# Optimization experiments

Hardware: AMD Instinct MI355X
Metric: run time of the kernel (lower is better)

## Reference

```python
import jax, jax.numpy as jnp
import numpy as np

B, S, D, H, NH, C = 32, 512, 768, 768, 4, 10
HD = H // NH


def _lin(x, w, b):
    return x @ w.T + b


def _ln(x, g, b, eps=1e-5):
    mu = jnp.mean(x, axis=-1, keepdims=True)
    var = jnp.mean(jnp.square(x - mu), axis=-1, keepdims=True)
    return (x - mu) * jax.lax.rsqrt(var + eps) * g + b


def setup_inputs() -> dict:
    key = jax.random.key(0)
    ks = jax.random.split(key, 16)
    w = lambda k, shape: jax.random.normal(k, shape, dtype=jnp.float32) * 0.02
    return {
        "x": jax.random.normal(ks[0], (B, S, D), dtype=jnp.float32),
        "wq": w(ks[1], (H, D)), "bq": jnp.zeros((H,), jnp.float32),
        "wk": w(ks[2], (H, D)), "bk": jnp.zeros((H,), jnp.float32),
        "wv": w(ks[3], (H, D)), "bv": jnp.zeros((H,), jnp.float32),
        "wx": w(ks[4], (H, D)), "bx": jnp.zeros((H,), jnp.float32),
        "in_proj_w": w(ks[5], (3 * H, H)), "in_proj_b": jnp.zeros((3 * H,), jnp.float32),
        "out_proj_w": w(ks[6], (H, H)), "out_proj_b": jnp.zeros((H,), jnp.float32),
        "fc1a_w": w(ks[7], (H, H)), "fc1a_b": jnp.zeros((H,), jnp.float32),
        "fc1b_w": w(ks[8], (H, H)), "fc1b_b": jnp.zeros((H,), jnp.float32),
        "ln_g": jnp.ones((H,), jnp.float32), "ln_b": jnp.zeros((H,), jnp.float32),
        "fc2_w": w(ks[9], (C, H)), "fc2_b": jnp.zeros((C,), jnp.float32),
    }


def reference(x, wq, bq, wk, bk, wv, bv, wx, bx, in_proj_w, in_proj_b,
              out_proj_w, out_proj_b, fc1a_w, fc1a_b, fc1b_w, fc1b_b,
              ln_g, ln_b, fc2_w, fc2_b):
    # Vectorized sinusoidal PE matching the triple loop:
    # even i: sin(pos / 10000^(2i/D)); odd i: cos(pos / 10000^(2(i-1)/D))
    d = x.shape[2]
    pos = jnp.arange(x.shape[1], dtype=x.dtype)[:, None]          # [S,1]
    i = jnp.arange(d)
    i_even = (i - (i % 2)).astype(x.dtype)                        # 2*(i - i%2)/d exponent
    angle = pos / jnp.power(jnp.asarray(10000.0, x.dtype), 2.0 * i_even / d)  # [S,D]
    pe = jnp.where(i % 2 == 0, jnp.sin(angle), jnp.cos(angle))
    x = x + pe[None]

    q = _lin(x, wq, bq)
    k = _lin(x, wk, bk)
    v = _lin(x, wv, bv)
    xr = _lin(x, wx, bx)

    # torch MultiheadAttention: in_proj, split heads, SDPA, out_proj
    wq_i, wk_i, wv_i = jnp.split(in_proj_w, 3, axis=0)
    bq_i, bk_i, bv_i = jnp.split(in_proj_b, 3, axis=0)
    b = x.shape[0]
    q2 = _lin(q, wq_i, bq_i).reshape(b, -1, NH, HD)
    k2 = _lin(k, wk_i, bk_i).reshape(b, -1, NH, HD)
    v2 = _lin(v, wv_i, bv_i).reshape(b, -1, NH, HD)
    scores = jnp.einsum('bqhd,bkhd->bhqk', q2, k2) / jnp.sqrt(jnp.asarray(HD, x.dtype))
    attn = jax.nn.softmax(scores, axis=-1)
    ctx = jnp.einsum('bhqk,bkhd->bqhd', attn, v2).reshape(b, -1, H)
    attn_out = _lin(ctx, out_proj_w, out_proj_b)

    x = _ln(xr + attn_out, ln_g, ln_b)
    ffn = _lin(jax.nn.relu(_lin(x, fc1a_w, fc1a_b)), fc1b_w, fc1b_b)
    x = _ln(x + ffn, ln_g, ln_b)
    x = jnp.sum(x, axis=1)
    return _lin(x, fc2_w, fc2_b)
```

## Files before the change

kernel.cpp:

```cpp
#include <hip/hip_runtime.h>
#include <hip/hip_bf16.h>

typedef __bf16 bf16;
typedef __bf16 bf16x8 __attribute__((ext_vector_type(8)));
typedef __bf16 bf16x4 __attribute__((ext_vector_type(4)));
typedef __bf16 bf16x2 __attribute__((ext_vector_type(2)));
typedef float  f32x4  __attribute__((ext_vector_type(4)));

#define GLD16(g, l) __builtin_amdgcn_global_load_lds(                        \
    (const __attribute__((address_space(1))) void*)(g),                      \
    (__attribute__((address_space(3))) void*)(l), 16, 0, 0)

template<int BM, int BN, int MFR, int NFR>
__global__ __launch_bounds__(256, 3)
void gemm_nt(const bf16* __restrict__ A, const bf16* __restrict__ B,
             bf16* __restrict__ C, const float* __restrict__ bias,
             int K, int lda, int ldb, int ldc,
             int inner,
             long long aOut, long long aIn,
             long long bOut, long long bIn,
             long long cOut, long long cIn,
             float alpha, int relu,
             const bf16* __restrict__ res, int ldr)
{
    const int z  = blockIdx.z;
    const int zo = z / inner;
    const int zi = z - zo * inner;
    A += (long long)zo * aOut + (long long)zi * aIn;
    B += (long long)zo * bOut + (long long)zi * bIn;
    C += (long long)zo * cOut + (long long)zi * cIn;

    const int tm = blockIdx.y * BM;
    const int tn = blockIdx.x * BN;

    __shared__ __align__(16) bf16 smem[(BM + BN) * 64];
    bf16* As = smem;
    bf16* Bs = smem + BM * 64;

    const int tid  = threadIdx.x;
    const int lane = tid & 63;
    const int wid  = tid >> 6;
    const int wr   = wid >> 1;
    const int wc   = wid & 1;

    f32x4 acc[MFR][NFR];
#pragma unroll
    for (int i = 0; i < MFR; ++i)
#pragma unroll
        for (int j = 0; j < NFR; ++j) acc[i][j] = (f32x4){0.f, 0.f, 0.f, 0.f};

    const int srow = lane >> 3;
    const int gch8 = ((lane & 7) ^ srow) * 8;

    const int NA = BM / 32;
    const int NB = BN / 32;

    const bf16* aP[NA];
#pragma unroll
    for (int jj = 0; jj < NA; ++jj) {
        const int R0 = (wid * NA + jj) * 8;
        aP[jj] = A + (long long)(tm + R0 + srow) * lda + gch8;
    }
    const bf16* bP[NB];
#pragma unroll
    for (int jj = 0; jj < NB; ++jj) {
        const int R0 = (wid * NB + jj) * 8;
        bP[jj] = B + (long long)(tn + R0 + srow) * ldb + gch8;
    }

    const int lr = lane & 15;
    const int qg = lane >> 4;

    for (int kt = 0; kt < K; kt += 64) {
#pragma unroll
        for (int jj = 0; jj < NA; ++jj)
            GLD16(aP[jj], As + (wid * NA + jj) * 512);
#pragma unroll
        for (int jj = 0; jj < NB; ++jj)
            GLD16(bP[jj], Bs + (wid * NB + jj) * 512);
        __syncthreads();

#pragma unroll
        for (int h = 0; h < 2; ++h) {
            const int off = ((qg + h * 4) ^ (lr & 7)) * 8;
            bf16x8 af[MFR], bfr[NFR];
#pragma unroll
            for (int i = 0; i < MFR; ++i)
                af[i] = *(const bf16x8*)(As + (wr * MFR * 16 + i * 16 + lr) * 64 + off);
#pragma unroll
            for (int j = 0; j < NFR; ++j)
                bfr[j] = *(const bf16x8*)(Bs + (wc * NFR * 16 + j * 16 + lr) * 64 + off);
#pragma unroll
            for (int i = 0; i < MFR; ++i)
#pragma unroll
                for (int j = 0; j < NFR; ++j)
                    acc[i][j] = __builtin_amdgcn_mfma_f32_16x16x32_bf16(
                        af[i], bfr[j], acc[i][j], 0, 0, 0);
        }
        __syncthreads();
#pragma unroll
        for (int jj = 0; jj < NA; ++jj) aP[jj] += 64;
#pragma unroll
        for (int jj = 0; jj < NB; ++jj) bP[jj] += 64;
    }

#pragma unroll
    for (int i = 0; i < MFR; ++i) {
#pragma unroll
        for (int j = 0; j < NFR; ++j) {
            const int mm0 = tm + wr * MFR * 16 + i * 16 + (lane >> 4) * 4;
            const int nn  = tn + wc * NFR * 16 + j * 16 + (lane & 15);
#pragma unroll
            for (int r = 0; r < 4; ++r) {
                float v = acc[i][j][r] * alpha;
                if (bias) v += bias[nn];
                if (res)  v += (float)res[(long long)(mm0 + r) * ldr + nn];
                if (relu) v = fmaxf(v, 0.f);
                C[(long long)(mm0 + r) * ldc + nn] = (bf16)v;
            }
        }
    }
}

#define BAR8()  __builtin_amdgcn_s_barrier()
#define LGKM0() do { asm volatile("s_waitcnt lgkmcnt(0)" ::: "memory");      \
                     __builtin_amdgcn_sched_barrier(0); } while (0)

#define RD_A(S, MB)                                                          \
    _Pragma("unroll") for (int mi = 0; mi < 4; ++mi)                         \
    _Pragma("unroll") for (int h = 0; h < 2; ++h)                            \
        af[mi][h] = *(const bf16x8*)((S) + aBase + ((MB) + mi) * 1024 +      \
                                     (h ? koff1 : koff0));

#define RD_B(S, NJ)                                                          \
    _Pragma("unroll") for (int h = 0; h < 2; ++h)                            \
        bfv[NJ][h] = *(const bf16x8*)((S) + bBase + (NJ) * 1024 +            \
                                      (h ? koff1 : koff0));

#define MFMA_Q(MB, N0, N1)                                                   \
    __builtin_amdgcn_s_setprio(1);                                          \
    _Pragma("unroll") for (int h = 0; h < 2; ++h)                            \
    _Pragma("unroll") for (int mi = 0; mi < 4; ++mi) {                       \
        acc[(MB)+mi][(N0)] = __builtin_amdgcn_mfma_f32_16x16x32_bf16(        \
            af[mi][h], bfv[(N0)][h], acc[(MB)+mi][(N0)], 0, 0, 0);           \
        acc[(MB)+mi][(N1)] = __builtin_amdgcn_mfma_f32_16x16x32_bf16(        \
            af[mi][h], bfv[(N1)][h], acc[(MB)+mi][(N1)], 0, 0, 0);           \
    }                                                                        \
    __builtin_amdgcn_s_setprio(0);

#define MFMA_Q1(MB, N0)                                                      \
    __builtin_amdgcn_s_setprio(1);                                          \
    _Pragma("unroll") for (int h = 0; h < 2; ++h)                            \
    _Pragma("unroll") for (int mi = 0; mi < 4; ++mi) {                       \
        acc[(MB)+mi][(N0)] = __builtin_amdgcn_mfma_f32_16x16x32_bf16(        \
            af[mi][h], bfv[(N0)][h], acc[(MB)+mi][(N0)], 0, 0, 0);           \
    }                                                                        \
    __builtin_amdgcn_s_setprio(0);

#define STAGE_A(DST)                                                         \
    _Pragma("unroll") for (int jj = 0; jj < 4; ++jj) {                       \
        GLD16(aP[jj], (DST) + (wid * 4 + jj) * 512);  aP[jj] += 64; }

#define STAGE_B(DST)                                                         \
    _Pragma("unroll") for (int jj = 0; jj < 4; ++jj) {                       \
        GLD16(bP[jj], (DST) + 16384 + (wid * 4 + jj) * 512);  bP[jj] += 64; }

#define STAGE_B3(DST)                                                        \
    _Pragma("unroll") for (int jj = 0; jj < 3; ++jj) {                       \
        GLD16(bP[jj], (DST) + 16384 + (wid * 3 + jj) * 512);  bP[jj] += 64; }

#define K_TILE_F(CUR, NXT, STG, LAST)                                        \
  {                                                                          \
    RD_A((CUR), 0); RD_B((CUR), 0); RD_B((CUR), 1);                          \
    if (STG) { STAGE_A(NXT) }                                                \
    LGKM0();                                                                 \
    MFMA_Q(0, 0, 1)                                                          \
    RD_B((CUR), 2); RD_B((CUR), 3);                                          \
    if (STG) { STAGE_B(NXT) }                                                \
    LGKM0();                                                                 \
    MFMA_Q(0, 2, 3)                                                          \
    RD_A((CUR), 4);                                                          \
    LGKM0();                                                                 \
    MFMA_Q(4, 2, 3)                                                          \
    MFMA_Q(4, 0, 1)                                                          \
    if (!(LAST)) { asm volatile("s_waitcnt vmcnt(0)" ::: "memory");          \
                   __builtin_amdgcn_sched_barrier(0); BAR8(); }              \
  }

#define K_TILE_F3(CUR, NXT, STG, LAST)                                       \
  {                                                                          \
    RD_A((CUR), 0); RD_B((CUR), 0); RD_B((CUR), 1);                          \
    if (STG) { STAGE_A(NXT) }                                                \
    LGKM0();                                                                 \
    MFMA_Q(0, 0, 1)                                                          \
    RD_B((CUR), 2);                                                          \
    if (STG) { STAGE_B3(NXT) }                                               \
    LGKM0();                                                                 \
    MFMA_Q1(0, 2)                                                            \
    RD_A((CUR), 4);                                                          \
    LGKM0();                                                                 \
    MFMA_Q1(4, 2)                                                            \
    MFMA_Q(4, 0, 1)                                                          \
    if (!(LAST)) { asm volatile("s_waitcnt vmcnt(0)" ::: "memory");          \
                   __builtin_amdgcn_sched_barrier(0); BAR8(); }              \
  }

__global__ __launch_bounds__(512, 2)
void gemm_qkv_8ph(const bf16* __restrict__ A, const bf16* __restrict__ B,
                  bf16* __restrict__ C, const float* __restrict__ bias)
{
    constexpr int LDA = 768, LDB = 768, LDC = 3072;
    const int tm = blockIdx.y * 256;
    const int tn = blockIdx.x * 256;

    __shared__ __align__(16) bf16 smem[2][2 * 256 * 64];

    const int tid  = threadIdx.x;
    const int lane = tid & 63;
    const int wid  = tid >> 6;
    const int wr   = wid >> 2;
    const int wc   = wid & 3;
    const int lr   = lane & 15;
    const int qg   = lane >> 4;

    const int srow = lane >> 3;
    const int gch8 = ((lane & 7) ^ srow) * 8;
    const bf16* aP[4];
    const bf16* bP[4];
#pragma unroll
    for (int jj = 0; jj < 4; ++jj) {
        aP[jj] = A + (long long)(tm + wid * 32 + jj * 8 + srow) * LDA + gch8;
        bP[jj] = B + (long long)(tn + wid * 32 + jj * 8 + srow) * LDB + gch8;
    }

    f32x4 acc[8][4];
#pragma unroll
    for (int i = 0; i < 8; ++i)
#pragma unroll
        for (int j = 0; j < 4; ++j) acc[i][j] = (f32x4){0.f, 0.f, 0.f, 0.f};

    const int aBase = (wr * 128 + lr) * 64;
    const int bBase = 16384 + (wc * 64 + lr) * 64;
    const int koff0 = ((qg    ) ^ (lr & 7)) * 8;
    const int koff1 = ((qg + 4) ^ (lr & 7)) * 8;

    bf16x8 af[4][2];
    bf16x8 bfv[4][2];

    bf16* S0 = &smem[0][0];
    bf16* S1 = &smem[1][0];

    STAGE_A(S0)
    STAGE_B(S0)
    asm volatile("s_waitcnt vmcnt(0)" ::: "memory");
    BAR8();

#pragma unroll 1
    for (int it = 0; it < 5; ++it) {
        K_TILE_F(S0, S1, 1, 0)
        K_TILE_F(S1, S0, 1, 0)
    }
    K_TILE_F(S0, S1, 1, 0)
    K_TILE_F(S1, S0, 0, 1)

    float bv[4];
#pragma unroll
    for (int j = 0; j < 4; ++j) bv[j] = bias[tn + wc * 64 + j * 16 + lr];

#pragma unroll
    for (int i = 0; i < 8; ++i) {
        const int mm0 = tm + wr * 128 + i * 16 + qg * 4;
#pragma unroll
        for (int j = 0; j < 4; ++j) {
            const int nn = tn + wc * 64 + j * 16 + lr;
#pragma unroll
            for (int r = 0; r < 4; ++r)
                C[(long long)(mm0 + r) * LDC + nn] = (bf16)(acc[i][j][r] + bv[j]);
        }
    }
}

__global__ __launch_bounds__(512, 2)
void gemm_flow(const bf16* __restrict__ A, const bf16* __restrict__ B,
               bf16* __restrict__ C, const float* __restrict__ bias,
               int lda, int ldb, int ldc, int relu,
               const bf16* __restrict__ res, int ldr)
{
    const int tm = blockIdx.y * 256;
    const int tn = blockIdx.x * 192;

    __shared__ __align__(16) bf16 smem[2][(256 + 192) * 64];

    const int tid  = threadIdx.x;
    const int lane = tid & 63;
    const int wid  = tid >> 6;
    const int wr   = wid >> 2;
    const int wc   = wid & 3;
    const int lr   = lane & 15;
    const int qg   = lane >> 4;

    const int srow = lane >> 3;
    const int gch8 = ((lane & 7) ^ srow) * 8;
    const bf16* aP[4];
    const bf16* bP[3];
#pragma unroll
    for (int jj = 0; jj < 4; ++jj)
        aP[jj] = A + (long long)(tm + wid * 32 + jj * 8 + srow) * lda + gch8;
#pragma unroll
    for (int jj = 0; jj < 3; ++jj)
        bP[jj] = B + (long long)(tn + wid * 24 + jj * 8 + srow) * ldb + gch8;

    f32x4 acc[8][3];
#pragma unroll
    for (int i = 0; i < 8; ++i)
#pragma unroll
        for (int j = 0; j < 3; ++j) acc[i][j] = (f32x4){0.f, 0.f, 0.f, 0.f};

    const int aBase = (wr * 128 + lr) * 64;
    const int bBase = 16384 + (wc * 48 + lr) * 64;
    const int koff0 = ((qg    ) ^ (lr & 7)) * 8;
    const int koff1 = ((qg + 4) ^ (lr & 7)) * 8;

    bf16x8 af[4][2];
    bf16x8 bfv[3][2];

    bf16* S0 = &smem[0][0];
    bf16* S1 = &smem[1][0];

    STAGE_A(S0)
    STAGE_B3(S0)
    asm volatile("s_waitcnt vmcnt(0)" ::: "memory");
    BAR8();

#pragma unroll 1
    for (int it = 0; it < 5; ++it) {
        K_TILE_F3(S0, S1, 1, 0)
        K_TILE_F3(S1, S0, 1, 0)
    }
    K_TILE_F3(S0, S1, 1, 0)
    K_TILE_F3(S1, S0, 0, 1)

    float bv[3];
#pragma unroll
    for (int j = 0; j < 3; ++j) bv[j] = bias ? bias[tn + wc * 48 + j * 16 + lr] : 0.f;

#pragma unroll
    for (int i = 0; i < 8; ++i) {
        const int mm0 = tm + wr * 128 + i * 16 + qg * 4;
#pragma unroll
        for (int j = 0; j < 3; ++j) {
            const int nn = tn + wc * 48 + j * 16 + lr;
#pragma unroll
            for (int r = 0; r < 4; ++r) {
                float v = acc[i][j][r] + bv[j];
                if (res)  v += (float)res[(long long)(mm0 + r) * ldr + nn];
                if (relu) v = fmaxf(v, 0.f);
                C[(long long)(mm0 + r) * ldc + nn] = (bf16)v;
            }
        }
    }
}

__global__ __launch_bounds__(256, 2)
void fused_attn_kernel(bf16* __restrict__ qkvx)
{
    const int flat = blockIdx.x;
    const int qt = (flat >> 3) & 3;
    const int z  = (flat & 7) | ((flat >> 5) << 3);
    const int b  = z >> 2, h = z & 3;

    const bf16* Qg = qkvx + (long long)b * 512 * 3072 + h * 192;
    const bf16* Kg = Qg + 768;
    const bf16* Vg = Qg + 1536;

    __shared__ __align__(16) bf16 Ks[64 * 192];
    __shared__ __align__(16) bf16 VTs[192 * 64];
    __shared__ __align__(16) bf16 Pb[4 * 32 * 64];

    const int tid  = threadIdx.x;
    const int lane = tid & 63;
    const int wid  = tid >> 6;
    const int lr   = lane & 15;
    const int qg   = lane >> 4;
    const int m0   = qt * 128 + wid * 32;

    bf16x8 qf[2][6];
#pragma unroll
    for (int mt = 0; mt < 2; ++mt)
#pragma unroll
        for (int t = 0; t < 6; ++t)
            qf[mt][t] = *(const bf16x8*)(Qg + (long long)(m0 + mt * 16 + lr) * 3072
                                         + t * 32 + qg * 8);

    const bf16* kP[6];
#pragma unroll
    for (int i = 0; i < 6; ++i) {
        const int c = i * 256 + tid;
        const int krow = c / 24, kcc = c % 24;
        const int kgc  = (kcc & 24) | ((kcc & 7) ^ (krow & 7));
        kP[i] = Kg + (long long)krow * 3072 + kgc * 8;
    }
    const int vkp = tid & 31;
    const int vdc = tid >> 5;

    f32x4 acc[2][12];
#pragma unroll
    for (int mt = 0; mt < 2; ++mt)
#pragma unroll
        for (int dt = 0; dt < 12; ++dt) acc[mt][dt] = (f32x4){0.f, 0.f, 0.f, 0.f};
    float mrow[2][4], lrow[2][4];
#pragma unroll
    for (int mt = 0; mt < 2; ++mt)
#pragma unroll
        for (int r = 0; r < 4; ++r) { mrow[mt][r] = -3e38f; lrow[mt][r] = 0.f; }

    const float alpha = 0.0721687836f;

    for (int kt = 0; kt < 8; ++kt) {
#pragma unroll
        for (int i = 0; i < 6; ++i)
            GLD16(kP[i], Ks + (i * 256 + wid * 64) * 8);
#pragma unroll
        for (int i = 0; i < 3; ++i) {
            const int dc = vdc + i * 8;
            const bf16* p = Vg + (long long)(2 * vkp) * 3072 + dc * 8;
            const bf16x8 v0 = *(const bf16x8*)(p);
            const bf16x8 v1 = *(const bf16x8*)(p + 3072);
#pragma unroll
            for (int j = 0; j < 8; ++j) {
                const int d = dc * 8 + j;
                bf16x2 pk; pk[0] = v0[j]; pk[1] = v1[j];
                *(bf16x2*)(VTs + d * 64 + ((vkp >> 2) ^ (d & 7)) * 8
                           + 2 * (vkp & 3)) = pk;
            }
        }
        __syncthreads();

        f32x4 sf[2][4];
#pragma unroll
        for (int mt = 0; mt < 2; ++mt)
#pragma unroll
            for (int nt = 0; nt < 4; ++nt) sf[mt][nt] = (f32x4){0.f, 0.f, 0.f, 0.f};
#pragma unroll
        for (int nt = 0; nt < 4; ++nt) {
#pragma unroll
            for (int t = 0; t < 6; ++t) {
                const int ch = t * 4 + qg;
                const int ph = (ch & 24) | ((ch & 7) ^ (lr & 7));
                const bf16x8 kf = *(const bf16x8*)(Ks + (nt * 16 + lr) * 192 + ph * 8);
                sf[0][nt] = __builtin_amdgcn_mfma_f32_16x16x32_bf16(qf[0][t], kf, sf[0][nt], 0, 0, 0);
                sf[1][nt] = __builtin_amdgcn_mfma_f32_16x16x32_bf16(qf[1][t], kf, sf[1][nt], 0, 0, 0);
            }
        }

#pragma unroll
        for (int mt = 0; mt < 2; ++mt) {
            float mx[4], a[4], rs[4], p[4][4];
#pragma unroll
            for (int r = 0; r < 4; ++r) {
                float v0 = fmaxf(sf[mt][0][r], sf[mt][1][r]);
                float v1 = fmaxf(sf[mt][2][r], sf[mt][3][r]);
                mx[r] = fmaxf(v0, v1) * alpha;
            }
#pragma unroll
            for (int msk = 1; msk <= 8; msk <<= 1)
#pragma unroll
                for (int r = 0; r < 4; ++r) mx[r] = fmaxf(mx[r], __shfl_xor(mx[r], msk));
#pragma unroll
            for (int r = 0; r < 4; ++r) {
                const float mn = fmaxf(mrow[mt][r], mx[r]);
                a[r] = __expf(mrow[mt][r] - mn);
                mrow[mt][r] = mn;
                rs[r] = 0.f;
            }
#pragma unroll
            for (int nt = 0; nt < 4; ++nt)
#pragma unroll
                for (int r = 0; r < 4; ++r) {
                    p[nt][r] = __expf(sf[mt][nt][r] * alpha - mrow[mt][r]);
                    rs[r] += p[nt][r];
                }
#pragma unroll
            for (int msk = 1; msk <= 8; msk <<= 1)
#pragma unroll
                for (int r = 0; r < 4; ++r) rs[r] += __shfl_xor(rs[r], msk);
#pragma unroll
            for (int r = 0; r < 4; ++r) lrow[mt][r] = lrow[mt][r] * a[r] + rs[r];
#pragma unroll
            for (int dt = 0; dt < 12; ++dt)
#pragma unroll
                for (int r = 0; r < 4; ++r) acc[mt][dt][r] *= a[r];
#pragma unroll
            for (int nt = 0; nt < 4; ++nt)
#pragma unroll
                for (int r = 0; r < 4; ++r) {
                    const int row = mt * 16 + qg * 4 + r;
                    const int ph2 = (nt * 2 + (lr >> 3)) ^ (row & 7);
                    Pb[wid * 2048 + row * 64 + ph2 * 8 + (lr & 7)] = (bf16)p[nt][r];
                }
        }

        bf16x8 pf[2][2];
#pragma unroll
        for (int mt = 0; mt < 2; ++mt)
#pragma unroll
            for (int ks = 0; ks < 2; ++ks) {
                const int row = mt * 16 + lr;
                const int ph  = (ks * 4 + qg) ^ (lr & 7);
                pf[mt][ks] = *(const bf16x8*)(Pb + wid * 2048 + row * 64 + ph * 8);
            }
#pragma unroll
        for (int dt = 0; dt < 12; ++dt) {
#pragma unroll
            for (int ks = 0; ks < 2; ++ks) {
                const int ph = (ks * 4 + qg) ^ (lr & 7);
                const bf16x8 vf = *(const bf16x8*)(VTs + (dt * 16 + lr) * 64 + ph * 8);
                acc[0][dt] = __builtin_amdgcn_mfma_f32_16x16x32_bf16(pf[0][ks], vf, acc[0][dt], 0, 0, 0);
                acc[1][dt] = __builtin_amdgcn_mfma_f32_16x16x32_bf16(pf[1][ks], vf, acc[1][dt], 0, 0, 0);
            }
        }
        __syncthreads();
#pragma unroll
        for (int i = 0; i < 6; ++i) kP[i] += 64 * 3072;
        Vg += 64 * 3072;
    }

    bf16* Og = qkvx + (long long)b * 512 * 3072 + h * 192;
#pragma unroll
    for (int mt = 0; mt < 2; ++mt) {
        float inv[4];
#pragma unroll
        for (int r = 0; r < 4; ++r) inv[r] = 1.0f / lrow[mt][r];
#pragma unroll
        for (int dt = 0; dt < 12; ++dt)
#pragma unroll
            for (int r = 0; r < 4; ++r) {
                const int row = m0 + mt * 16 + qg * 4 + r;
                Og[(long long)row * 3072 + dt * 16 + lr] = (bf16)(acc[mt][dt][r] * inv[r]);
            }
    }
}

__device__ __forceinline__ void cast4(const float* src, bf16* dst, int i)
{
    const float4 v = *(const float4*)(src + (long long)i * 4);
    bf16x4 o;
    o[0] = (bf16)v.x; o[1] = (bf16)v.y; o[2] = (bf16)v.z; o[3] = (bf16)v.w;
    *(bf16x4*)(dst + (long long)i * 4) = o;
}

__global__ __launch_bounds__(256)
void prep_kernel(const float* __restrict__ wq, const float* __restrict__ wk,
                 const float* __restrict__ wv, const float* __restrict__ wx,
                 const float* __restrict__ inpw, const float* __restrict__ inpb,
                 const float* __restrict__ bq, const float* __restrict__ bk,
                 const float* __restrict__ bv, const float* __restrict__ bx,
                 const float* __restrict__ woutp, const float* __restrict__ wf1a,
                 const float* __restrict__ wf1b, const float* __restrict__ x,
                 bf16* __restrict__ WT3, bf16* __restrict__ INPJ,
                 bf16* __restrict__ WOUT, bf16* __restrict__ WF1A,
                 bf16* __restrict__ WF1B, bf16* __restrict__ WXD,
                 float* __restrict__ BCAT, bf16* __restrict__ XPE)
{
    const int blk = blockIdx.x;
    const int tid = threadIdx.x;
    __shared__ bf16 t[32][33];

    if (blk < 1728) {
        const int which = blk / 576, local = blk - which * 576;
        const float* src = (which == 0) ? wq : ((which == 1) ? wk : wv);
        bf16* dst = WT3 + (long long)which * 589824;
        const int r0 = (local / 24) * 32, c0 = (local % 24) * 32;
        const int tr = tid >> 5, tc = tid & 31;
#pragma unroll
        for (int k = 0; k < 4; ++k) {
            const int r = tr + k * 8;
            t[r][tc] = (bf16)src[(long long)(r0 + r) * 768 + c0 + tc];
        }
        __syncthreads();
#pragma unroll
        for (int k = 0; k < 4; ++k) {
            const int c = tr + k * 8;
            dst[(long long)(c0 + c) * 768 + r0 + tc] = t[tc][c];
        }
    } else if (blk < 3456) {
        cast4(inpw, INPJ, (blk - 1728) * 256 + tid);
    } else if (blk < 4032) {
        cast4(woutp, WOUT, (blk - 3456) * 256 + tid);
    } else if (blk < 4608) {
        cast4(wf1a, WF1A, (blk - 4032) * 256 + tid);
    } else if (blk < 5184) {
        cast4(wf1b, WF1B, (blk - 4608) * 256 + tid);
    } else if (blk < 5760) {
        cast4(wx, WXD, (blk - 5184) * 256 + tid);
    } else if (blk < 6051) {
        const int bl = blk - 5760;
        if (bl < 288) {
            const int g = tid >> 5, l = tid & 31;
            const int n = bl * 8 + g;
            const int zsec = n / 768;
            const float* bb = (zsec == 0) ? bq : ((zsec == 1) ? bk : bv);
            const float* wrow = inpw + (long long)n * 768;
            float s = 0.f;
            for (int d = l; d < 768; d += 32) s += wrow[d] * bb[d];
#pragma unroll
            for (int off = 16; off; off >>= 1) s += __shfl_xor(s, off);
            if (l == 0) BCAT[n] = inpb[n] + s;
        } else {
            const int n = (bl - 288) * 256 + tid;
            if (n < 768) BCAT[2304 + n] = bx[n];
        }
    } else {
        const int idx4 = ((blk - 6051) * 256 + tid) * 4;
        const int d    = idx4 % 768;
        const int row  = idx4 / 768;
        const int s    = row & 511;
        const float ksc = -0.034603417655076f;
        const float4 xv = *(const float4*)(x + (long long)idx4);
        float a0 = (float)s * exp2f((float)d * ksc);
        float a1 = (float)s * exp2f((float)(d + 2) * ksc);
        float s0, c0, s1, c1;
        sincosf(a0, &s0, &c0);
        sincosf(a1, &s1, &c1);
        bf16x4 o;
        o[0] = (bf16)(xv.x + s0);
        o[1] = (bf16)(xv.y + c0);
        o[2] = (bf16)(xv.z + s1);
        o[3] = (bf16)(xv.w + c1);
        *(bf16x4*)(XPE + (long long)idx4) = o;
    }
}

__global__ __launch_bounds__(192)
void ln1_kernel(const bf16* __restrict__ a, int lda_,
                bf16* __restrict__ o, int ldo,
                const float* __restrict__ g, const float* __restrict__ be)
{
    const int row = blockIdx.x;
    const int t   = threadIdx.x;
    const int d0  = t * 4;
    const bf16x4 av = *(const bf16x4*)(a + (long long)row * lda_ + d0);
    float xv[4];
#pragma unroll
    for (int k = 0; k < 4; ++k) xv[k] = (float)av[k];
    float s1 = xv[0] + xv[1] + xv[2] + xv[3];
    float s2 = xv[0]*xv[0] + xv[1]*xv[1] + xv[2]*xv[2] + xv[3]*xv[3];
    for (int off = 32; off; off >>= 1) {
        s1 += __shfl_xor(s1, off);
        s2 += __shfl_xor(s2, off);
    }
    __shared__ float red[6];
    const int wid = t >> 6, lane = t & 63;
    if (lane == 0) { red[wid] = s1; red[3 + wid] = s2; }
    __syncthreads();
    s1 = red[0] + red[1] + red[2];
    s2 = red[3] + red[4] + red[5];
    const float mu  = s1 * (1.0f / 768.0f);
    const float var = s2 * (1.0f / 768.0f) - mu * mu;
    const float rs  = rsqrtf(var + 1e-5f);
    const float4 gv = *(const float4*)(g + d0);
    const float4 ev = *(const float4*)(be + d0);
    bf16x4 ov;
    ov[0] = (bf16)(((xv[0] - mu) * rs) * gv.x + ev.x);
    ov[1] = (bf16)(((xv[1] - mu) * rs) * gv.y + ev.y);
    ov[2] = (bf16)(((xv[2] - mu) * rs) * gv.z + ev.z);
    ov[3] = (bf16)(((xv[3] - mu) * rs) * gv.w + ev.w);
    *(bf16x4*)(o + (long long)row * ldo + d0) = ov;
}

__global__ __launch_bounds__(256)
void ln2_reduce_kernel(const bf16* __restrict__ src,
                       const float* __restrict__ g, const float* __restrict__ be,
                       float* __restrict__ partial)
{
    const int blk  = blockIdx.x;
    const int tid  = threadIdx.x;
    const int wid  = tid >> 6, lane = tid & 63;
    const int d0   = lane * 12;

    float gv[12], ev[12];
#pragma unroll
    for (int k = 0; k < 12; k += 4) {
        *(float4*)(gv + k) = *(const float4*)(g + d0 + k);
        *(float4*)(ev + k) = *(const float4*)(be + d0 + k);
    }
    float acc[12];
#pragma unroll
    for (int k = 0; k < 12; ++k) acc[k] = 0.f;

    for (int i = 0; i < 8; ++i) {
        const int row = blk * 32 + i * 4 + wid;
        const bf16* p = src + (long long)row * 3072 + d0;
        float xv[12];
#pragma unroll
        for (int k = 0; k < 12; k += 4) {
            const bf16x4 v = *(const bf16x4*)(p + k);
            xv[k] = (float)v[0]; xv[k+1] = (float)v[1];
            xv[k+2] = (float)v[2]; xv[k+3] = (float)v[3];
        }
        float s1 = 0.f, s2 = 0.f;
#pragma unroll
        for (int k = 0; k < 12; ++k) { s1 += xv[k]; s2 += xv[k] * xv[k]; }
        for (int off = 32; off; off >>= 1) {
            s1 += __shfl_xor(s1, off);
            s2 += __shfl_xor(s2, off);
        }
        const float mu  = s1 * (1.0f / 768.0f);
        const float var = s2 * (1.0f / 768.0f) - mu * mu;
        const float rs  = rsqrtf(var + 1e-5f);
#pragma unroll
        for (int k = 0; k < 12; ++k) acc[k] += (xv[k] - mu) * rs * gv[k] + ev[k];
    }

    __shared__ float red[4][768];
#pragma unroll
    for (int k = 0; k < 12; k += 4)
        *(float4*)(&red[wid][d0 + k]) = *(const float4*)(acc + k);
    __syncthreads();
    if (wid == 0) {
#pragma unroll
        for (int k = 0; k < 12; k += 4) {
            const float4 a0 = *(const float4*)(&red[0][d0 + k]);
            const float4 a1 = *(const float4*)(&red[1][d0 + k]);
            const float4 a2 = *(const float4*)(&red[2][d0 + k]);
            const float4 a3 = *(const float4*)(&red[3][d0 + k]);
            *(float4*)(partial + (long long)blk * 768 + d0 + k) =
                make_float4(a0.x + a1.x + a2.x + a3.x, a0.y + a1.y + a2.y + a3.y,
                            a0.z + a1.z + a2.z + a3.z, a0.w + a1.w + a2.w + a3.w);
        }
    }
}

__global__ __launch_bounds__(192)
void reduce_fc2_stage2_kernel(const float* __restrict__ partial, const float* __restrict__ w,
                              const float* __restrict__ bias, float* __restrict__ out)
{
    const int b = blockIdx.x, t = threadIdx.x;
    const int d0 = t * 4;
    float a[4] = {0.f, 0.f, 0.f, 0.f};
    for (int c = 0; c < 16; ++c) {
        const float4 pv = *(const float4*)(partial + (long long)(b * 16 + c) * 768 + d0);
        a[0] += pv.x; a[1] += pv.y; a[2] += pv.z; a[3] += pv.w;
    }
    __shared__ float os[10];
    if (t < 10) os[t] = 0.f;
    __syncthreads();
    for (int c = 0; c < 10; ++c) {
        const float4 wv = *(const float4*)(w + c * 768 + d0);
        float p = wv.x * a[0] + wv.y * a[1] + wv.z * a[2] + wv.w * a[3];
        for (int off = 32; off; off >>= 1) p += __shfl_xor(p, off);
        if ((t & 63) == 0) atomicAdd(&os[c], p);
    }
    __syncthreads();
    if (t < 10) out[b * 10 + t] = os[t] + bias[t];
}

static const size_t OFF_XPE  = 0;
static const size_t OFF_WCAT = OFF_XPE  + (size_t)16384 * 768 * 2;
static const size_t OFF_WT3  = OFF_WCAT + (size_t)3072 * 768 * 2;
static const size_t OFF_INPJ = OFF_WT3  + (size_t)3 * 768 * 768 * 2;
static const size_t OFF_WOUT = OFF_INPJ + (size_t)2304 * 768 * 2;
static const size_t OFF_WF1A = OFF_WOUT + (size_t)768 * 768 * 2;
static const size_t OFF_WF1B = OFF_WF1A + (size_t)768 * 768 * 2;
static const size_t OFF_BCAT = OFF_WF1B + (size_t)768 * 768 * 2;
static const size_t OFF_QKVX = OFF_BCAT + (size_t)3072 * 4;
static const size_t OFF_VT   = OFF_QKVX + (size_t)16384 * 3072 * 2;
static const size_t OFF_S    = OFF_VT   + (size_t)128 * 192 * 512 * 2;
static const size_t OFF_X1   = OFF_S    + (size_t)128 * 512 * 512 * 2;

extern "C" void kernel_launch(void* const* d_in, const int* in_sizes, int n_in,
                              void* d_out, int out_size, void* d_ws, size_t ws_size,
                              hipStream_t stream)
{
    const float* x     = (const float*)d_in[0];
    const float* wq    = (const float*)d_in[1];
    const float* bq    = (const float*)d_in[2];
    const float* wk    = (const float*)d_in[3];
    const float* bk    = (const float*)d_in[4];
    const float* wv    = (const float*)d_in[5];
    const float* bv    = (const float*)d_in[6];
    const float* wx    = (const float*)d_in[7];
    const float* bx    = (const float*)d_in[8];
    const float* inpw  = (const float*)d_in[9];
    const float* inpb  = (const float*)d_in[10];
    const float* woutp = (const float*)d_in[11];
    const float* boutp = (const float*)d_in[12];
    const float* wf1a  = (const float*)d_in[13];
    const float* bf1a  = (const float*)d_in[14];
    const float* wf1b  = (const float*)d_in[15];
    const float* bf1b  = (const float*)d_in[16];
    const float* lng   = (const float*)d_in[17];
    const float* lnb   = (const float*)d_in[18];
    const float* wfc2  = (const float*)d_in[19];
    const float* bfc2  = (const float*)d_in[20];
    float* out = (float*)d_out;

    char* ws = (char*)d_ws;
    bf16*  XPE  = (bf16*)(ws + OFF_XPE);
    bf16*  WCAT = (bf16*)(ws + OFF_WCAT);
    bf16*  WT3  = (bf16*)(ws + OFF_WT3);
    bf16*  INPJ = (bf16*)(ws + OFF_INPJ);
    bf16*  WOUT = (bf16*)(ws + OFF_WOUT);
    bf16*  WF1A = (bf16*)(ws + OFF_WF1A);
    bf16*  WF1B = (bf16*)(ws + OFF_WF1B);
    float* BCAT = (float*)(ws + OFF_BCAT);
    bf16*  QKVX = (bf16*)(ws + OFF_QKVX);
    float* PART = (float*)(ws + OFF_S);
    bf16*  X1   = (bf16*)(ws + OFF_X1);

    prep_kernel<<<18339, 256, 0, stream>>>(wq, wk, wv, wx, inpw, inpb,
                                           bq, bk, bv, bx, woutp, wf1a, wf1b, x,
                                           WT3, INPJ, WOUT, WF1A, WF1B,
                                           WCAT + (size_t)2304 * 768, BCAT, XPE);

    gemm_nt<64, 128, 2, 4><<<dim3(6, 12, 3), 256, 0, stream>>>(
        INPJ, WT3, WCAT, nullptr, 768, 768, 768, 768,
        1, 589824, 0, 589824, 0, 589824, 0, 1.0f, 0, nullptr, 0);

    gemm_qkv_8ph<<<dim3(12, 64, 1), 512, 0, stream>>>(XPE, WCAT, QKVX, BCAT);

    fused_attn_kernel<<<512, 256, 0, stream>>>(QKVX);

    gemm_flow<<<dim3(4, 64, 1), 512, 0, stream>>>(
        QKVX, WOUT, QKVX + 768, boutp, 3072, 768, 3072,
        0, QKVX + 2304, 3072);

    ln1_kernel<<<16384, 192, 0, stream>>>(QKVX + 768, 3072, X1, 768, lng, lnb);

    gemm_flow<<<dim3(4, 64, 1), 512, 0, stream>>>(
        X1, WF1A, QKVX + 1536, bf1a, 768, 768, 3072,
        1, nullptr, 0);

    gemm_flow<<<dim3(4, 64, 1), 512, 0, stream>>>(
        QKVX + 1536, WF1B, QKVX + 2304, bf1b, 3072, 768, 3072,
        0, X1, 768);

    ln2_reduce_kernel<<<512, 256, 0, stream>>>(QKVX + 2304, lng, lnb, PART);

    reduce_fc2_stage2_kernel<<<32, 192, 0, stream>>>(PART, wfc2, bfc2, out);
}
```

Before: 444.8 us.

## Alias attention P buffer onto K tile and batch LN1 rows per wave

```diff
diff --git a/kernel.cpp b/kernel.cpp
--- a/kernel.cpp
+++ b/kernel.cpp
@@ -375,7 +375,7 @@
 
     __shared__ __align__(16) bf16 Ks[64 * 192];
     __shared__ __align__(16) bf16 VTs[192 * 64];
-    __shared__ __align__(16) bf16 Pb[4 * 32 * 64];
+    bf16* const Pb = Ks;
 
     const int tid  = threadIdx.x;
     const int lane = tid & 63;
@@ -452,6 +452,9 @@
                 sf[1][nt] = __builtin_amdgcn_mfma_f32_16x16x32_bf16(qf[1][t], kf, sf[1][nt], 0, 0, 0);
             }
         }
+        asm volatile("s_waitcnt lgkmcnt(0)" ::: "memory");
+        __builtin_amdgcn_s_barrier();
+        __builtin_amdgcn_sched_barrier(0);
 
 #pragma unroll
         for (int mt = 0; mt < 2; ++mt) {
@@ -631,41 +634,54 @@
     }
 }
 
-__global__ __launch_bounds__(192)
+__global__ __launch_bounds__(256)
 void ln1_kernel(const bf16* __restrict__ a, int lda_,
                 bf16* __restrict__ o, int ldo,
                 const float* __restrict__ g, const float* __restrict__ be)
 {
-    const int row = blockIdx.x;
-    const int t   = threadIdx.x;
-    const int d0  = t * 4;
-    const bf16x4 av = *(const bf16x4*)(a + (long long)row * lda_ + d0);
-    float xv[4];
-#pragma unroll
-    for (int k = 0; k < 4; ++k) xv[k] = (float)av[k];
-    float s1 = xv[0] + xv[1] + xv[2] + xv[3];
-    float s2 = xv[0]*xv[0] + xv[1]*xv[1] + xv[2]*xv[2] + xv[3]*xv[3];
-    for (int off = 32; off; off >>= 1) {
-        s1 += __shfl_xor(s1, off);
-        s2 += __shfl_xor(s2, off);
-    }
-    __shared__ float red[6];
-    const int wid = t >> 6, lane = t & 63;
-    if (lane == 0) { red[wid] = s1; red[3 + wid] = s2; }
-    __syncthreads();
-    s1 = red[0] + red[1] + red[2];
-    s2 = red[3] + red[4] + red[5];
-    const float mu  = s1 * (1.0f / 768.0f);
-    const float var = s2 * (1.0f / 768.0f) - mu * mu;
-    const float rs  = rsqrtf(var + 1e-5f);
-    const float4 gv = *(const float4*)(g + d0);
-    const float4 ev = *(const float4*)(be + d0);
-    bf16x4 ov;
-    ov[0] = (bf16)(((xv[0] - mu) * rs) * gv.x + ev.x);
-    ov[1] = (bf16)(((xv[1] - mu) * rs) * gv.y + ev.y);
-    ov[2] = (bf16)(((xv[2] - mu) * rs) * gv.z + ev.z);
-    ov[3] = (bf16)(((xv[3] - mu) * rs) * gv.w + ev.w);
-    *(bf16x4*)(o + (long long)row * ldo + d0) = ov;
+    const int blk  = blockIdx.x;
+    const int tid  = threadIdx.x;
+    const int wid  = tid >> 6, lane = tid & 63;
+    const int d0   = lane * 12;
+
+    float gv[12], ev[12];
+#pragma unroll
+    for (int k = 0; k < 12; k += 4) {
+        *(float4*)(gv + k) = *(const float4*)(g + d0 + k);
+        *(float4*)(ev + k) = *(const float4*)(be + d0 + k);
+    }
+
+    for (int i = 0; i < 8; ++i) {
+        const int row = blk * 32 + i * 4 + wid;
+        const bf16* p = a + (long long)row * lda_ + d0;
+        float xv[12];
+#pragma unroll
+        for (int k = 0; k < 12; k += 4) {
+            const bf16x4 v = *(const bf16x4*)(p + k);
+            xv[k] = (float)v[0]; xv[k+1] = (float)v[1];
+            xv[k+2] = (float)v[2]; xv[k+3] = (float)v[3];
+        }
+        float s1 = 0.f, s2 = 0.f;
+#pragma unroll
+        for (int k = 0; k < 12; ++k) { s1 += xv[k]; s2 += xv[k] * xv[k]; }
+        for (int off = 32; off; off >>= 1) {
+            s1 += __shfl_xor(s1, off);
+            s2 += __shfl_xor(s2, off);
+        }
+        const float mu  = s1 * (1.0f / 768.0f);
+        const float var = s2 * (1.0f / 768.0f) - mu * mu;
+        const float rs  = rsqrtf(var + 1e-5f);
+        bf16* po = o + (long long)row * ldo + d0;
+#pragma unroll
+        for (int k = 0; k < 12; k += 4) {
+            bf16x4 ov;
+            ov[0] = (bf16)((xv[k]   - mu) * rs * gv[k]   + ev[k]);
+            ov[1] = (bf16)((xv[k+1] - mu) * rs * gv[k+1] + ev[k+1]);
+            ov[2] = (bf16)((xv[k+2] - mu) * rs * gv[k+2] + ev[k+2]);
+            ov[3] = (bf16)((xv[k+3] - mu) * rs * gv[k+3] + ev[k+3]);
+            *(bf16x4*)(po + k) = ov;
+        }
+    }
 }
 
 __global__ __launch_bounds__(256)
@@ -825,7 +841,7 @@
         QKVX, WOUT, QKVX + 768, boutp, 3072, 768, 3072,
         0, QKVX + 2304, 3072);
 
-    ln1_kernel<<<16384, 192, 0, stream>>>(QKVX + 768, 3072, X1, 768, lng, lnb);
+    ln1_kernel<<<512, 256, 0, stream>>>(QKVX + 768, 3072, X1, 768, lng, lnb);
 
     gemm_flow<<<dim3(4, 64, 1), 512, 0, stream>>>(
         X1, WF1A, QKVX + 1536, bf1a, 768, 768, 3072,
```

Result: slower. 454.5 us (+2.2%).
